# Optimization experiments

Hardware: AMD Instinct MI355X
Metric: run time of the kernel (lower is better)

The kernel has to match this reference:

```python
import jax, jax.numpy as jnp
import numpy as np

# dims
D_MODEL = 256; D_STATE = 16; D_CONV = 4; EXPAND = 2
D_INNER = D_MODEL * EXPAND            # 512
DT_RANK = 16                          # ceil(256/16)
B_SZ = 16; C_IN = 64; T_LR = 2560; R = 2; C_OUT = 64


def _p(key, shape, scale=0.02):
    return jax.random.normal(key, shape, jnp.float32) * scale


def setup_inputs() -> dict:
    key = jax.random.key(0)
    ks = iter(jax.random.split(key, 48))
    inp = {}
    inp['x'] = jax.random.normal(next(ks), (B_SZ, C_IN, T_LR), jnp.float32)
    # encoder: Conv1d(64->128,k3,p1) ; Conv1d(128->256,k3,p1)
    inp['enc_w1'] = _p(next(ks), (128, C_IN, 3)); inp['enc_b1'] = jnp.zeros((128,), jnp.float32)
    inp['enc_w2'] = _p(next(ks), (256, 128, 3)); inp['enc_b2'] = jnp.zeros((256,), jnp.float32)
    # BidirectionalMamba norms
    inp['norm1_w'] = jnp.ones((D_MODEL,), jnp.float32)
    inp['norm2_w'] = jnp.ones((D_MODEL,), jnp.float32)
    # one forward ('f') and one backward ('b') Mamba v1 block
    for p in ('f', 'b'):
        inp[p + '_inW'] = _p(next(ks), (2 * D_INNER, D_MODEL))
        inp[p + '_convW'] = _p(next(ks), (D_INNER, D_CONV), 0.2)
        inp[p + '_convb'] = jnp.zeros((D_INNER,), jnp.float32)
        inp[p + '_xW'] = _p(next(ks), (DT_RANK + 2 * D_STATE, D_INNER))
        inp[p + '_dtW'] = _p(next(ks), (D_INNER, DT_RANK), 0.1)
        inp[p + '_dtb'] = -4.0 + 2.0 * jax.random.uniform(next(ks), (D_INNER,), jnp.float32)
        inp[p + '_Alog'] = jnp.log(jnp.tile(jnp.arange(1, D_STATE + 1, dtype=jnp.float32), (D_INNER, 1)))
        inp[p + '_D'] = jnp.ones((D_INNER,), jnp.float32)
        inp[p + '_outW'] = _p(next(ks), (D_MODEL, D_INNER))
    # post-bottleneck: Conv1d(512->256,k3,p1) + BatchNorm1d(256) (eval)
    inp['convd_w'] = _p(next(ks), (256, 512, 3)); inp['convd_b'] = jnp.zeros((256,), jnp.float32)
    inp['bn_g'] = jnp.ones((256,), jnp.float32); inp['bn_b'] = jnp.zeros((256,), jnp.float32)
    inp['bn_mean'] = jnp.zeros((256,), jnp.float32); inp['bn_var'] = jnp.ones((256,), jnp.float32)
    # SubPixel1D: Conv1d(256 -> target_channels*r, k3, p1), r=2
    inp['sp_w'] = _p(next(ks), (C_OUT * R, 256, 3)); inp['sp_b'] = jnp.zeros((C_OUT * R,), jnp.float32)
    return inp


def silu(x):
    return x * jax.nn.sigmoid(x)


def conv1d(x, w, b):  # x: (B,C,L), w: (O,I,K), 'same' padding
    k = w.shape[-1]
    y = jax.lax.conv_general_dilated(x, w, (1,), [(k // 2, k // 2)],
                                     dimension_numbers=('NCH', 'OIH', 'NCH'))
    return y + b[None, :, None]


def rmsnorm(x, w, eps=1e-6):
    return x * jax.lax.rsqrt(jnp.mean(x * x, -1, keepdims=True) + eps) * w


def mamba(x, inW, convW, convb, xW, dtW, dtb, Alog, Dp, outW):
    # x: (B, L, D_MODEL) -> (B, L, D_MODEL); Mamba v1 selective scan.
    Bn = x.shape[0]
    xz = x @ inW.T                               # (B,L,2*di)
    xc, z = jnp.split(xz, 2, axis=-1)            # (B,L,di) each
    # causal depthwise conv over time
    xt = jnp.transpose(xc, (0, 2, 1))            # (B,di,L)
    xt = jax.lax.conv_general_dilated(xt, convW[:, None, :], (1,), [(D_CONV - 1, 0)],
                                      dimension_numbers=('NCH', 'OIH', 'NCH'),
                                      feature_group_count=D_INNER)
    xc = silu(jnp.transpose(xt + convb[None, :, None], (0, 2, 1)))  # (B,L,di)
    dbc = xc @ xW.T                              # (B,L,dt_rank+2N)
    dt = jax.nn.softplus(dbc[..., :DT_RANK] @ dtW.T + dtb)          # (B,L,di)
    Bc = dbc[..., DT_RANK:DT_RANK + D_STATE]     # (B,L,N)
    Cc = dbc[..., DT_RANK + D_STATE:]            # (B,L,N)
    A = -jnp.exp(Alog)                           # (di,N)

    def step(h, inp):
        dt_t, B_t, C_t, x_t = inp                # (B,di),(B,N),(B,N),(B,di)
        dA = jnp.exp(dt_t[..., None] * A)        # (B,di,N)
        h = dA * h + (dt_t * x_t)[..., None] * B_t[:, None, :]
        y = jnp.einsum('bdn,bn->bd', h, C_t)
        return h, y

    xs = (jnp.transpose(dt, (1, 0, 2)), jnp.transpose(Bc, (1, 0, 2)),
          jnp.transpose(Cc, (1, 0, 2)), jnp.transpose(xc, (1, 0, 2)))
    h0 = jnp.zeros((Bn, D_INNER, D_STATE), x.dtype)
    _, ys = jax.lax.scan(step, h0, xs)           # ys: (L,B,di)
    y = jnp.transpose(ys, (1, 0, 2)) + xc * Dp
    return (y * silu(z)) @ outW.T


def reference(x, enc_w1, enc_b1, enc_w2, enc_b2, norm1_w, norm2_w,
              f_inW, f_convW, f_convb, f_xW, f_dtW, f_dtb, f_Alog, f_D, f_outW,
              b_inW, b_convW, b_convb, b_xW, b_dtW, b_dtb, b_Alog, b_D, b_outW,
              convd_w, convd_b, bn_g, bn_b, bn_mean, bn_var, sp_w, sp_b):
    # encoder (dropout = identity in eval)
    e = silu(conv1d(x, enc_w1, enc_b1))
    e = silu(conv1d(e, enc_w2, enc_b2))          # (B,256,T)
    t = jnp.transpose(e, (0, 2, 1))              # (B,T,256)
    # Bi-Mamba bottleneck layer
    xn = rmsnorm(t, norm1_w)
    mo_f = mamba(xn, f_inW, f_convW, f_convb, f_xW, f_dtW, f_dtb, f_Alog, f_D, f_outW) + xn
    xb = xn[:, ::-1, :]
    mo_b = mamba(xb, b_inW, b_convW, b_convb, b_xW, b_dtW, b_dtb, b_Alog, b_D, b_outW) + xb
    mo_b = mo_b[:, ::-1, :]
    combined = rmsnorm(mo_f + mo_b, norm2_w)
    m = jnp.concatenate([combined, t], axis=-1)  # (B,T,512)
    m = jnp.transpose(m, (0, 2, 1))              # (B,512,T)
    # conv_d + BatchNorm1d (eval) + SiLU
    d = conv1d(m, convd_w, convd_b)
    d = (d - bn_mean[None, :, None]) * jax.lax.rsqrt(bn_var + 1e-5)[None, :, None] \
        * bn_g[None, :, None] + bn_b[None, :, None]
    d = silu(d)
    # SubPixel1D upsample x2
    s = conv1d(d, sp_w, sp_b)                    # (B, C_OUT*R, T)
    Bn, C, T = s.shape
    s = s.reshape(Bn, C // R, R, T).transpose(0, 1, 3, 2).reshape(Bn, C // R, T * R)
    return s                                      # (B, 64, 5120)
```

## Files before the change

### kernel.cpp

```cpp
#include <hip/hip_runtime.h>
#include <hip/hip_bf16.h>
#include <math.h>

#define B_SZ 16
#define T_LR 2560
#define BT (B_SZ * T_LR)
#define DM 256
#define DI 512
#define DS 16
#define DTR 16
#define CH 64
#define CH_LOG2 6
#define CLEN (T_LR / CH)

typedef __attribute__((ext_vector_type(8))) short bf16x8;
typedef __attribute__((ext_vector_type(4))) float f32x4;

__device__ __forceinline__ float silu_f(float x) {
    return x / (1.f + __expf(-x));
}
__device__ __forceinline__ unsigned short f2bf(float v) {
    __hip_bfloat16 h = __float2bfloat16(v);
    return *(unsigned short*)&h;
}
__device__ __forceinline__ float bf2f(unsigned short u) {
    union { unsigned int i; float f; } c;
    c.i = (unsigned int)u << 16;
    return c.f;
}
__device__ __forceinline__ int seqrev(int r) {
    int s = r / T_LR, t = r % T_LR;
    return s * T_LR + (T_LR - 1 - t);
}
__device__ __forceinline__ float softplus_f(float x) {
    return (x > 20.f) ? x : __logf(1.f + __expf(x));
}
__device__ __forceinline__ size_t wswz_idx(int tap, int n, int c, int N, int Kt) {
    return ((size_t)((tap * (N >> 4) + (n >> 4)) * (Kt >> 5) + (c >> 5)) << 9)
         + (size_t)((((c >> 3) & 3) * 16 + (n & 15)) * 8 + (c & 7));
}

__global__ __launch_bounds__(256) void k_prep(
    const float* __restrict__ enc_w1, const float* __restrict__ enc_w2,
    const float* __restrict__ convd_w, const float* __restrict__ sp_w,
    const float* __restrict__ convd_b, const float* __restrict__ bn_g,
    const float* __restrict__ bn_b, const float* __restrict__ bn_mean,
    const float* __restrict__ bn_var,
    const float* __restrict__ inW0, const float* __restrict__ inW1,
    const float* __restrict__ outW0, const float* __restrict__ outW1,
    const float* __restrict__ xW0, const float* __restrict__ xW1,
    const float* __restrict__ Alog0, const float* __restrict__ Alog1,
    const float* __restrict__ x,
    unsigned short* __restrict__ W1r, unsigned short* __restrict__ W2r,
    unsigned short* __restrict__ Wdr, unsigned short* __restrict__ Wspr,
    float* __restrict__ alpha, float* __restrict__ beta,
    unsigned short* __restrict__ inW_bf2, unsigned short* __restrict__ outW_bf2,
    unsigned short* __restrict__ xW_bc2, float* __restrict__ Aflag,
    unsigned short* __restrict__ xt)
{
    __shared__ float ts[32][33];
    __shared__ int s_ok;
    int blk = blockIdx.x;
    int tid = threadIdx.x;
    if (blk < 32) {
        int i = blk * 256 + tid;
        int n = i / 64, ci = i % 64;
        #pragma unroll
        for (int k = 0; k < 3; k++)
            W1r[wswz_idx(k, n, ci, 128, 64)] = f2bf(enc_w1[((size_t)n * 64 + ci) * 3 + k]);
    } else if (blk < 160) {
        int i = (blk - 32) * 256 + tid;
        int n = i / 128, ci = i % 128;
        #pragma unroll
        for (int k = 0; k < 3; k++)
            W2r[wswz_idx(k, n, ci, 256, 128)] = f2bf(enc_w2[((size_t)n * 128 + ci) * 3 + k]);
    } else if (blk < 672) {
        int i = (blk - 160) * 256 + tid;
        int n = i / 512, ci = i % 512;
        #pragma unroll
        for (int k = 0; k < 3; k++)
            Wdr[wswz_idx(k, n, ci, 256, 512)] = f2bf(convd_w[((size_t)n * 512 + ci) * 3 + k]);
    } else if (blk < 800) {
        int i = (blk - 672) * 256 + tid;
        int n = i / 256, ci = i % 256;
        #pragma unroll
        for (int k = 0; k < 3; k++)
            Wspr[wswz_idx(k, n, ci, 128, 256)] = f2bf(sp_w[((size_t)n * 256 + ci) * 3 + k]);
    } else if (blk < 801) {
        int c = tid;
        float a = bn_g[c] * rsqrtf(bn_var[c] + 1e-5f);
        alpha[c] = a;
        beta[c] = (convd_b[c] - bn_mean[c]) * a + bn_b[c];
    } else if (blk < 1825) {
        int i = (blk - 801) * 256 + tid;
        inW_bf2[i] = f2bf(inW0[i]);
        inW_bf2[262144 + i] = f2bf(inW1[i]);
    } else if (blk < 2337) {
        int i = (blk - 1825) * 256 + tid;
        outW_bf2[i] = f2bf(outW0[i]);
        outW_bf2[131072 + i] = f2bf(outW1[i]);
    } else if (blk < 2433) {
        int i = (blk - 2337) * 256 + tid;
        xW_bc2[i] = f2bf(xW0[i]);
        xW_bc2[24576 + i] = f2bf(xW1[i]);
    } else if (blk < 2434) {
        if (tid == 0) s_ok = 1;
        __syncthreads();
        int ok = 1;
        for (int i = tid; i < DI * DS; i += 256) {
            int d = i >> 4, n = i & 15;
            float a0f = __expf(Alog0[d * DS]);
            float anf = __expf(Alog0[d * DS + n]);
            if (fabsf(anf - (float)(n + 1) * a0f) > 1e-3f * (float)(n + 1)) ok = 0;
            float a0b = __expf(Alog1[d * DS]);
            float anb = __expf(Alog1[d * DS + n]);
            if (fabsf(anb - (float)(n + 1) * a0b) > 1e-3f * (float)(n + 1)) ok = 0;
        }
        if (!ok) atomicAnd(&s_ok, 0);
        __syncthreads();
        if (tid == 0) Aflag[0] = s_ok ? 1.f : 0.f;
    } else {
        int idx = blk - 2434;
        int t0 = (idx % 80) * 32;
        int c0 = ((idx / 80) & 1) * 32;
        int b = idx / 160;
        int tx = tid & 31, ty = tid >> 5;
        #pragma unroll
        for (int j = 0; j < 4; j++) {
            int c = c0 + ty + j * 8;
            ts[ty + j * 8][tx] = x[((size_t)b * 64 + c) * T_LR + t0 + tx];
        }
        __syncthreads();
        #pragma unroll
        for (int j = 0; j < 4; j++) {
            int t = t0 + ty + j * 8;
            xt[((size_t)b * T_LR + t) * 64 + c0 + tx] = f2bf(ts[tx][ty + j * 8]);
        }
    }
}

__global__ __launch_bounds__(256, 3) void k_conv3_bf(const unsigned short* __restrict__ A1, int K1,
                                                  const unsigned short* __restrict__ A2, int K2,
                                                  const unsigned short* __restrict__ Wz,
                                                  const float* __restrict__ alpha,
                                                  const float* __restrict__ beta,
                                                  float* __restrict__ outf,
                                                  unsigned short* __restrict__ outb,
                                                  int N, int dosilu, int pixsh) {
    int Kt = K1 + K2;
    __shared__ __align__(16) unsigned short smem[2 * 130 * 40];
    unsigned short (*As)[130][40] = (unsigned short (*)[130][40])smem;
    float* sC = (float*)smem;
    int tid = threadIdx.x;
    int wave = tid >> 6, lane = tid & 63;
    int wm = (wave >> 1) * 64, wn = (wave & 1) * 64;
    int m0 = blockIdx.x * 128, n0 = blockIdx.y * 128;
    int b = m0 / T_LR, t0 = m0 % T_LR;
    int q = lane >> 4, ml = lane & 15;
    int Nb16 = N >> 4, Kb32 = Kt >> 5;
    int nb0 = (n0 + wn) >> 4;
    const unsigned short* wl = Wz + (size_t)lane * 8;
    f32x4 acc[4][4] = {};
    int cq = tid & 3;
    int r0 = tid >> 2;
    int r1 = r0 + 64;
    int r2 = r0 + 128;
    bool has2 = (tid < 8);
    int ta0 = t0 - 1 + r0, ta1 = t0 - 1 + r1, ta2 = t0 - 1 + r2;
    bool va0 = (ta0 >= 0) && (ta0 < T_LR);
    bool va1 = (ta1 < T_LR);
    bool va2 = has2 && (ta2 < T_LR);
    uint4 v0, v1, v2;
    #define LOADA(vv, valid, t, col) { vv = make_uint4(0u,0u,0u,0u); if (valid) { \
        const unsigned short* src = ((col) < K1) \
            ? A1 + (size_t)(b * T_LR + (t)) * K1 + (col) \
            : A2 + (size_t)(b * T_LR + (t)) * K2 + ((col) - K1); \
        vv = *(const uint4*)src; } }
    LOADA(v0, va0, ta0, cq * 8);
    LOADA(v1, va1, ta1, cq * 8);
    LOADA(v2, va2, ta2, cq * 8);
    *(uint4*)&As[0][r0][cq * 8] = v0;
    *(uint4*)&As[0][r1][cq * 8] = v1;
    if (has2) *(uint4*)&As[0][r2][cq * 8] = v2;
    int nk = Kb32;
    for (int kk = 0; kk < nk; kk++) {
        __syncthreads();
        int cur = kk & 1;
        if (kk + 1 < nk) {
            int col = ((kk + 1) << 5) + cq * 8;
            LOADA(v0, va0, ta0, col);
            LOADA(v1, va1, ta1, col);
            LOADA(v2, va2, ta2, col);
        }
        #pragma unroll
        for (int tap = 0; tap < 3; tap++) {
            int tb = tap * Nb16 + nb0;
            bf16x8 bfr[4];
            #pragma unroll
            for (int ni = 0; ni < 4; ni++)
                bfr[ni] = *(const bf16x8*)(wl + ((size_t)((tb + ni) * Kb32 + kk) << 9));
            #pragma unroll
            for (int mi = 0; mi < 4; mi++) {
                bf16x8 af = *(const bf16x8*)&As[cur][wm + mi * 16 + ml + tap][q * 8];
                #pragma unroll
                for (int ni = 0; ni < 4; ni++)
                    acc[mi][ni] = __builtin_amdgcn_mfma_f32_16x16x32_bf16(af, bfr[ni], acc[mi][ni], 0, 0, 0);
            }
        }
        if (kk + 1 < nk) {
            *(uint4*)&As[cur ^ 1][r0][cq * 8] = v0;
            *(uint4*)&As[cur ^ 1][r1][cq * 8] = v1;
            if (has2) *(uint4*)&As[cur ^ 1][r2][cq * 8] = v2;
        }
    }
    #undef LOADA
    int rowoff = m0 - b * T_LR;
    #pragma unroll
    for (int p = 0; p < 4; p++) {
        __syncthreads();
        if ((wave >> 1) == (p >> 1)) {
            int mib = (p & 1) * 2;
            #pragma unroll
            for (int m2 = 0; m2 < 2; m2++) {
                int mi = mib + m2;
                int rl = mi * 16 + q * 4 - (p & 1) * 32;
                #pragma unroll
                for (int r = 0; r < 4; r++)
                    #pragma unroll
                    for (int ni = 0; ni < 4; ni++)
                        sC[(rl + r) * 140 + wn + ni * 16 + ml] = acc[mi][ni][r];
            }
        }
        __syncthreads();
        if (pixsh) {
            int row = tid & 31, c2g = tid >> 5;
            int t = rowoff + p * 32 + row;
            float* dst = outf + ((size_t)b * 64 * T_LR + t) * 2;
            #pragma unroll
            for (int j = 0; j < 8; j++) {
                int c2 = c2g + j * 8;
                float va = sC[row * 140 + 2 * c2]     + beta[2 * c2];
                float vb = sC[row * 140 + 2 * c2 + 1] + beta[2 * c2 + 1];
                *(float2*)&dst[(size_t)c2 * T_LR * 2] = make_float2(va, vb);
            }
        } else {
            #pragma unroll
            for (int gi = 0; gi < 2; gi++) {
                int g = tid + gi * 256;
                int row = g >> 4;
                int colg = (g & 15) * 8;
                int mr = m0 + p * 32 + row;
                const float* src = sC + row * 140 + colg;
                float vv[8];
                *(float4*)&vv[0] = *(const float4*)src;
                *(float4*)&vv[4] = *(const float4*)(src + 4);
                unsigned short ob[8];
                #pragma unroll
                for (int jj = 0; jj < 8; jj++) {
                    int col = n0 + colg + jj;
                    float a = alpha ? alpha[col] : 1.f;
                    float v = vv[jj] * a + beta[col];
                    if (dosilu) v = silu_f(v);
                    vv[jj] = v;
                    ob[jj] = f2bf(v);
                }
                if (outf) {
                    *(float4*)(outf + (size_t)mr * N + n0 + colg) = *(float4*)&vv[0];
                    *(float4*)(outf + (size_t)mr * N + n0 + colg + 4) = *(float4*)&vv[4];
                }
                if (outb)
                    *(uint4*)(outb + (size_t)mr * N + n0 + colg) = *(uint4*)ob;
            }
        }
    }
}

__global__ __launch_bounds__(256) void k_inproj_conv(const unsigned short* __restrict__ xn,
                                                     const unsigned short* __restrict__ inW2,
                                                     const float* __restrict__ cw0,
                                                     const float* __restrict__ cw1,
                                                     const float* __restrict__ cb0,
                                                     const float* __restrict__ cb1,
                                                     unsigned short* __restrict__ xcs,
                                                     long long dsXcs) {
    __shared__ unsigned short As[128][40];
    __shared__ unsigned short Bs[128][40];
    __shared__ unsigned short Ct[131][136];
    int dir = blockIdx.z;
    int arev = dir;
    const unsigned short* inW = inW2 + (size_t)dir * 1024 * DM;
    const float* cw = dir ? cw1 : cw0;
    const float* cb = dir ? cb1 : cb0;
    xcs += (size_t)dir * dsXcs;
    int tid = threadIdx.x;
    int wave = tid >> 6, lane = tid & 63;
    int wm = (wave >> 1) * 64, wn = (wave & 1) * 64;
    int m0 = blockIdx.x * 128, n0 = blockIdx.y * 128;
    int b = m0 / T_LR, t0 = m0 % T_LR;
    int sc = tid & 3, sr = tid >> 2;
    int ar0 = m0 + sr, ar1 = m0 + sr + 64;
    if (arev) { ar0 = seqrev(ar0); ar1 = seqrev(ar1); }
    const unsigned short* ap0 = xn + (size_t)ar0 * DM + sc * 8;
    const unsigned short* ap1 = xn + (size_t)ar1 * DM + sc * 8;
    const unsigned short* bp0 = inW + (size_t)(n0 + sr) * DM + sc * 8;
    const unsigned short* bp1 = inW + (size_t)(n0 + sr + 64) * DM + sc * 8;
    f32x4 acc[4][4] = {};
    int q = lane >> 4, ml = lane & 15;
    for (int k0 = 0; k0 < DM; k0 += 32) {
        uint4 a0 = *(const uint4*)(ap0 + k0);
        uint4 a1 = *(const uint4*)(ap1 + k0);
        uint4 b0 = *(const uint4*)(bp0 + k0);
        uint4 b1 = *(const uint4*)(bp1 + k0);
        __syncthreads();
        *(uint4*)&As[sr][sc * 8]      = a0;
        *(uint4*)&As[sr + 64][sc * 8] = a1;
        *(uint4*)&Bs[sr][sc * 8]      = b0;
        *(uint4*)&Bs[sr + 64][sc * 8] = b1;
        __syncthreads();
        bf16x8 af[4], bfr[4];
        #pragma unroll
        for (int mi = 0; mi < 4; mi++)
            af[mi] = *(const bf16x8*)&As[wm + mi * 16 + ml][q * 8];
        #pragma unroll
        for (int ni = 0; ni < 4; ni++)
            bfr[ni] = *(const bf16x8*)&Bs[wn + ni * 16 + ml][q * 8];
        #pragma unroll
        for (int mi = 0; mi < 4; mi++)
            #pragma unroll
            for (int ni = 0; ni < 4; ni++)
                acc[mi][ni] = __builtin_amdgcn_mfma_f32_16x16x32_bf16(af[mi], bfr[ni], acc[mi][ni], 0, 0, 0);
    }
    #pragma unroll
    for (int mi = 0; mi < 4; mi++)
        #pragma unroll
        for (int r = 0; r < 4; r++)
            #pragma unroll
            for (int ni = 0; ni < 4; ni++)
                Ct[3 + wm + mi * 16 + q * 4 + r][wn + ni * 16 + ml] = f2bf(acc[mi][ni][r]);
    for (int i = tid; i < 384; i += 256) {
        int hr = i >> 7, c = i & 127;
        int tr = t0 - 3 + hr;
        float v = 0.f;
        if (tr >= 0) {
            int src = b * T_LR + (arev ? (T_LR - 1 - tr) : tr);
            const unsigned short* xr = xn + (size_t)src * DM;
            const unsigned short* wr = inW + (size_t)(n0 + c) * DM;
            for (int k = 0; k < DM; k += 8) {
                uint4 xa = *(const uint4*)(xr + k);
                uint4 wa = *(const uint4*)(wr + k);
                const unsigned short* xs = (const unsigned short*)&xa;
                const unsigned short* wsp = (const unsigned short*)&wa;
                #pragma unroll
                for (int j = 0; j < 8; j++) v += bf2f(xs[j]) * bf2f(wsp[j]);
            }
        }
        Ct[hr][c] = f2bf(v);
    }
    __syncthreads();
    int col = tid & 127;
    int d = n0 + col;
    float w0 = cw[d * 4 + 0], w1 = cw[d * 4 + 1], w2 = cw[d * 4 + 2], w3 = cw[d * 4 + 3];
    float bi = cb[d];
    int rbase = tid >> 7;
    for (int j = 0; j < 64; j++) {
        int row = rbase + 2 * j;
        float v = bi + bf2f(Ct[row][col]) * w0 + bf2f(Ct[row + 1][col]) * w1
                     + bf2f(Ct[row + 2][col]) * w2 + bf2f(Ct[row + 3][col]) * w3;
        xcs[(size_t)(m0 + row) * DI + d] = f2bf(silu_f(v));
    }
}

__global__ __launch_bounds__(256) void k_rmsnorm(const float* __restrict__ in1,
                                                 const float* __restrict__ in2,
                                                 const float* __restrict__ w,
                                                 float* __restrict__ out,
                                                 unsigned short* __restrict__ out_bf,
                                                 int ntok) {
    int tok = (blockIdx.x * 256 + threadIdx.x) >> 6;
    int lane = threadIdx.x & 63;
    if (tok >= ntok) return;
    float4 v = ((const float4*)(in1 + (size_t)tok * DM))[lane];
    if (in2) {
        float4 u = ((const float4*)(in2 + (size_t)tok * DM))[lane];
        v.x += u.x; v.y += u.y; v.z += u.z; v.w += u.w;
    }
    float ss = v.x * v.x + v.y * v.y + v.z * v.z + v.w * v.w;
    #pragma unroll
    for (int off = 32; off > 0; off >>= 1) ss += __shfl_xor(ss, off);
    float sc = rsqrtf(ss * (1.f / 256.f) + 1e-6f);
    float4 wv = ((const float4*)w)[lane];
    float4 o;
    o.x = v.x * sc * wv.x; o.y = v.y * sc * wv.y;
    o.z = v.z * sc * wv.z; o.w = v.w * sc * wv.w;
    if (out) ((float4*)(out + (size_t)tok * DM))[lane] = o;
    if (out_bf) {
        ushort4 ob;
        ob.x = f2bf(o.x); ob.y = f2bf(o.y); ob.z = f2bf(o.z); ob.w = f2bf(o.w);
        ((ushort4*)(out_bf + (size_t)tok * DM))[lane] = ob;
    }
}

__global__ __launch_bounds__(256) void k_gemm_bf(const unsigned short* __restrict__ A, int lda, long long dsA,
                                                 const unsigned short* __restrict__ Bw, long long dsB,
                                                 float* Cf, long long dsCf, int ldc,
                                                 const float* __restrict__ res,
                                                 int K, int Nout, int crevmode) {
    __shared__ unsigned short As[128][40];
    __shared__ unsigned short Bs[128][40];
    int dir = blockIdx.z;
    A += (long long)dir * dsA;
    Bw += (long long)dir * dsB;
    Cf += (long long)dir * dsCf;
    int crev = (crevmode == 2) ? dir : crevmode;
    int tid = threadIdx.x;
    int wave = tid >> 6, lane = tid & 63;
    int wm = (wave >> 1) * 64, wn = (wave & 1) * 64;
    int m0 = blockIdx.x * 128, n0 = blockIdx.y * 128;
    int sc = tid & 3, sr = tid >> 2;
    const unsigned short* ap0 = A + (size_t)(m0 + sr) * lda + sc * 8;
    const unsigned short* ap1 = A + (size_t)(m0 + sr + 64) * lda + sc * 8;
    bool bv0 = (n0 + sr) < Nout;
    bool bv1 = (n0 + sr + 64) < Nout;
    const unsigned short* bp0 = Bw + (size_t)(n0 + sr) * K + sc * 8;
    const unsigned short* bp1 = Bw + (size_t)(n0 + sr + 64) * K + sc * 8;
    f32x4 acc[4][4] = {};
    int q = lane >> 4, ml = lane & 15;
    for (int k0 = 0; k0 < K; k0 += 32) {
        uint4 a0 = *(const uint4*)(ap0 + k0);
        uint4 a1 = *(const uint4*)(ap1 + k0);
        uint4 b0 = make_uint4(0u, 0u, 0u, 0u), b1 = make_uint4(0u, 0u, 0u, 0u);
        if (bv0) b0 = *(const uint4*)(bp0 + k0);
        if (bv1) b1 = *(const uint4*)(bp1 + k0);
        __syncthreads();
        *(uint4*)&As[sr][sc * 8]      = a0;
        *(uint4*)&As[sr + 64][sc * 8] = a1;
        *(uint4*)&Bs[sr][sc * 8]      = b0;
        *(uint4*)&Bs[sr + 64][sc * 8] = b1;
        __syncthreads();
        bf16x8 af[4], bfr[4];
        #pragma unroll
        for (int mi = 0; mi < 4; mi++)
            af[mi] = *(const bf16x8*)&As[wm + mi * 16 + ml][q * 8];
        #pragma unroll
        for (int ni = 0; ni < 4; ni++)
            bfr[ni] = *(const bf16x8*)&Bs[wn + ni * 16 + ml][q * 8];
        #pragma unroll
        for (int mi = 0; mi < 4; mi++)
            #pragma unroll
            for (int ni = 0; ni < 4; ni++)
                acc[mi][ni] = __builtin_amdgcn_mfma_f32_16x16x32_bf16(af[mi], bfr[ni], acc[mi][ni], 0, 0, 0);
    }
    #pragma unroll
    for (int mi = 0; mi < 4; mi++) {
        #pragma unroll
        for (int r = 0; r < 4; r++) {
            int mr = m0 + wm + mi * 16 + q * 4 + r;
            int orow = crev ? seqrev(mr) : mr;
            #pragma unroll
            for (int ni = 0; ni < 4; ni++) {
                int col = n0 + wn + ni * 16 + ml;
                if (col < Nout) {
                    float v = acc[mi][ni][r];
                    if (res) v += res[(size_t)orow * ldc + col];
                    Cf[(size_t)orow * ldc + col] = v;
                }
            }
        }
    }
}

__global__ __launch_bounds__(256) void k_gemm_bf_cb(const unsigned short* __restrict__ A, int lda,
                                                    const unsigned short* __restrict__ Bw, long long dsB,
                                                    unsigned short* __restrict__ Cb, int ldc, long long dsCb,
                                                    const unsigned short* __restrict__ gate, long long dsGate,
                                                    int K) {
    __shared__ __align__(16) unsigned short smem[2 * 128 * 40];
    unsigned short (*As)[40] = (unsigned short(*)[40])smem;
    unsigned short (*Bs)[40] = (unsigned short(*)[40])(smem + 128 * 40);
    float* sC = (float*)smem;
    int dir = blockIdx.z;
    int arev = dir;
    Bw += (long long)dir * dsB;
    Cb += (long long)dir * dsCb;
    gate += (long long)dir * dsGate;
    int tid = threadIdx.x;
    int wave = tid >> 6, lane = tid & 63;
    int wm = (wave >> 1) * 64, wn = (wave & 1) * 64;
    int m0 = blockIdx.x * 128, n0 = blockIdx.y * 128;
    int sc = tid & 3, sr = tid >> 2;
    int ar0 = m0 + sr, ar1 = m0 + sr + 64;
    if (arev) { ar0 = seqrev(ar0); ar1 = seqrev(ar1); }
    const unsigned short* ap0 = A + (size_t)ar0 * lda + sc * 8;
    const unsigned short* ap1 = A + (size_t)ar1 * lda + sc * 8;
    const unsigned short* bp0 = Bw + (size_t)(n0 + sr) * K + sc * 8;
    const unsigned short* bp1 = Bw + (size_t)(n0 + sr + 64) * K + sc * 8;
    f32x4 acc[4][4] = {};
    int q = lane >> 4, ml = lane & 15;
    for (int k0 = 0; k0 < K; k0 += 32) {
        uint4 a0 = *(const uint4*)(ap0 + k0);
        uint4 a1 = *(const uint4*)(ap1 + k0);
        uint4 b0 = *(const uint4*)(bp0 + k0);
        uint4 b1 = *(const uint4*)(bp1 + k0);
        __syncthreads();
        *(uint4*)&As[sr][sc * 8]      = a0;
        *(uint4*)&As[sr + 64][sc * 8] = a1;
        *(uint4*)&Bs[sr][sc * 8]      = b0;
        *(uint4*)&Bs[sr + 64][sc * 8] = b1;
        __syncthreads();
        bf16x8 af[4], bfr[4];
        #pragma unroll
        for (int mi = 0; mi < 4; mi++)
            af[mi] = *(const bf16x8*)&As[wm + mi * 16 + ml][q * 8];
        #pragma unroll
        for (int ni = 0; ni < 4; ni++)
            bfr[ni] = *(const bf16x8*)&Bs[wn + ni * 16 + ml][q * 8];
        #pragma unroll
        for (int mi = 0; mi < 4; mi++)
            #pragma unroll
            for (int ni = 0; ni < 4; ni++)
                acc[mi][ni] = __builtin_amdgcn_mfma_f32_16x16x32_bf16(af[mi], bfr[ni], acc[mi][ni], 0, 0, 0);
    }
    #pragma unroll
    for (int p = 0; p < 4; p++) {
        __syncthreads();
        if ((wave >> 1) == (p >> 1)) {
            int mib = (p & 1) * 2;
            #pragma unroll
            for (int m2 = 0; m2 < 2; m2++) {
                int mi = mib + m2;
                int rl = mi * 16 + q * 4 - (p & 1) * 32;
                #pragma unroll
                for (int r = 0; r < 4; r++)
                    #pragma unroll
                    for (int ni = 0; ni < 4; ni++)
                        sC[(rl + r) * 140 + wn + ni * 16 + ml] = acc[mi][ni][r];
            }
        }
        __syncthreads();
        #pragma unroll
        for (int gi = 0; gi < 2; gi++) {
            int g = tid + gi * 256;
            int row = g >> 4;
            int colg = (g & 15) * 8;
            int grow = m0 + p * 32 + row;
            const float* src = sC + row * 140 + colg;
            float4 v0 = *(const float4*)src;
            float4 v1 = *(const float4*)(src + 4);
            float vv[8] = {v0.x, v0.y, v0.z, v0.w, v1.x, v1.y, v1.z, v1.w};
            unsigned short gu[8];
            *(uint4*)gu = *(const uint4*)(gate + (size_t)grow * ldc + n0 + colg);
            unsigned short o[8];
            #pragma unroll
            for (int jj = 0; jj < 8; jj++) {
                float v = vv[jj];
                v = silu_f(v) * bf2f(gu[jj]);
                o[jj] = f2bf(v);
            }
            *(uint4*)(Cb + (size_t)grow * ldc + n0 + colg) = *(uint4*)o;
        }
    }
}

__global__ __launch_bounds__(256) void k_scan_p1(const unsigned short* __restrict__ x,
                                                 const float* __restrict__ db,
                                                 const float* __restrict__ dtW0, const float* __restrict__ dtW1,
                                                 const float* __restrict__ dtb0, const float* __restrict__ dtb1,
                                                 const float* __restrict__ Alog0, const float* __restrict__ Alog1,
                                                 const float* __restrict__ Aflag,
                                                 float* __restrict__ hS,
                                                 float* __restrict__ csum, int Bc) {
    __shared__ float dbs[CLEN * 48];
    int tid = threadIdx.x;
    int gid = blockIdx.x * 256 + tid;
    int d = gid & (DI - 1);
    int bcix = gid >> 9;
    int c = bcix & (CH - 1);
    int bl = bcix >> CH_LOG2;
    int dir = (bl >= Bc) ? 1 : 0;
    const float* dtW  = dir ? dtW1  : dtW0;
    const float* dtb  = dir ? dtb1  : dtb0;
    const float* Alog = dir ? Alog1 : Alog0;
    int tbase = c * CLEN;
    const float* dbp = db + ((size_t)bl * T_LR + tbase) * 48;
    for (int i = tid; i < (CLEN * 48) / 4; i += 256)
        *(float4*)&dbs[i * 4] = *(const float4*)(dbp + i * 4);
    bool fast = (Aflag[0] != 0.f);
    float A0 = -__expf(Alog[d * DS]);
    float Av[DS], h[DS];
    #pragma unroll
    for (int n = 0; n < DS; n++) h[n] = 0.f;
    if (!fast) {
        #pragma unroll
        for (int n = 0; n < DS; n++) Av[n] = -__expf(Alog[d * DS + n]);
    }
    const float4* wp = (const float4*)(dtW + d * 16);
    float4 w0 = wp[0], w1 = wp[1], w2 = wp[2], w3 = wp[3];
    float bias = dtb[d];
    const unsigned short* xp = x + ((size_t)bl * T_LR + tbase) * DI + d;
    float S = 0.f;
    __syncthreads();
    for (int t = 0; t < CLEN; t++) {
        const float* bc = dbs + t * 48;
        float dl = bias
            + bc[0] * w0.x + bc[1] * w0.y + bc[2] * w0.z + bc[3] * w0.w
            + bc[4] * w1.x + bc[5] * w1.y + bc[6] * w1.z + bc[7] * w1.w
            + bc[8] * w2.x + bc[9] * w2.y + bc[10] * w2.z + bc[11] * w2.w
            + bc[12] * w3.x + bc[13] * w3.y + bc[14] * w3.z + bc[15] * w3.w;
        float dtv = softplus_f(dl);
        float xv  = bf2f(xp[(size_t)t * DI]);
        float dtx = dtv * xv;
        S += dtv;
        if (fast) {
            float e1 = __expf(dtv * A0);
            float e = e1;
            #pragma unroll
            for (int n = 0; n < DS; n++) {
                h[n] = e * h[n] + dtx * bc[16 + n];
                e *= e1;
            }
        } else {
            #pragma unroll
            for (int n = 0; n < DS; n++)
                h[n] = __expf(dtv * Av[n]) * h[n] + dtx * bc[16 + n];
        }
    }
    float* hp = hS + (size_t)gid * DS;
    #pragma unroll
    for (int n = 0; n < DS; n++) hp[n] = h[n];
    csum[gid] = S;
}

__global__ __launch_bounds__(256) void k_scan_p2(float* __restrict__ hS,
                                                 const float* __restrict__ csum,
                                                 const float* __restrict__ Alog0,
                                                 const float* __restrict__ Alog1, int Bc) {
    int gid = blockIdx.x * 256 + threadIdx.x;
    int n = gid & (DS - 1);
    int d = (gid >> 4) & (DI - 1);
    int bl = gid >> 13;
    const float* Alog = (bl >= Bc) ? Alog1 : Alog0;
    float An = -__expf(Alog[d * DS + n]);
    float hs = 0.f;
    for (int c = 0; c < CH; c++) {
        size_t base = ((size_t)(bl * CH + c) * DI + d);
        float he = hS[base * DS + n];
        float S  = csum[base];
        hS[base * DS + n] = hs;
        hs = __expf(An * S) * hs + he;
    }
}

__global__ __launch_bounds__(256) void k_scan_p3(unsigned short* __restrict__ x,
                                                 const float* __restrict__ db,
                                                 const float* __restrict__ dtW0, const float* __restrict__ dtW1,
                                                 const float* __restrict__ dtb0, const float* __restrict__ dtb1,
                                                 const float* __restrict__ Alog0, const float* __restrict__ Alog1,
                                                 const float* __restrict__ Aflag,
                                                 const float* __restrict__ Dp0, const float* __restrict__ Dp1,
                                                 const float* __restrict__ hS, int Bc) {
    __shared__ float dbs[CLEN * 48];
    int tid = threadIdx.x;
    int gid = blockIdx.x * 256 + tid;
    int d = gid & (DI - 1);
    int bcix = gid >> 9;
    int c = bcix & (CH - 1);
    int bl = bcix >> CH_LOG2;
    int dir = (bl >= Bc) ? 1 : 0;
    const float* dtW  = dir ? dtW1  : dtW0;
    const float* dtb  = dir ? dtb1  : dtb0;
    const float* Alog = dir ? Alog1 : Alog0;
    const float* Dp   = dir ? Dp1   : Dp0;
    int tbase = c * CLEN;
    const float* dbp = db + ((size_t)bl * T_LR + tbase) * 48;
    for (int i = tid; i < (CLEN * 48) / 4; i += 256)
        *(float4*)&dbs[i * 4] = *(const float4*)(dbp + i * 4);
    bool fast = (Aflag[0] != 0.f);
    float A0 = -__expf(Alog[d * DS]);
    float Av[DS], h[DS];
    const float* hp = hS + (size_t)gid * DS;
    #pragma unroll
    for (int n = 0; n < DS; n++) h[n] = hp[n];
    if (!fast) {
        #pragma unroll
        for (int n = 0; n < DS; n++) Av[n] = -__expf(Alog[d * DS + n]);
    }
    const float4* wp = (const float4*)(dtW + d * 16);
    float4 w0 = wp[0], w1 = wp[1], w2 = wp[2], w3 = wp[3];
    float bias = dtb[d];
    float Dd = Dp[d];
    unsigned short* xp = x + ((size_t)bl * T_LR + tbase) * DI + d;
    __syncthreads();
    for (int t = 0; t < CLEN; t++) {
        const float* bc = dbs + t * 48;
        float dl = bias
            + bc[0] * w0.x + bc[1] * w0.y + bc[2] * w0.z + bc[3] * w0.w
            + bc[4] * w1.x + bc[5] * w1.y + bc[6] * w1.z + bc[7] * w1.w
            + bc[8] * w2.x + bc[9] * w2.y + bc[10] * w2.z + bc[11] * w2.w
            + bc[12] * w3.x + bc[13] * w3.y + bc[14] * w3.z + bc[15] * w3.w;
        float dtv = softplus_f(dl);
        float xv  = bf2f(xp[(size_t)t * DI]);
        float dtx = dtv * xv;
        float acc = 0.f;
        if (fast) {
            float e1 = __expf(dtv * A0);
            float e = e1;
            #pragma unroll
            for (int n = 0; n < DS; n++) {
                h[n] = e * h[n] + dtx * bc[16 + n];
                acc += h[n] * bc[32 + n];
                e *= e1;
            }
        } else {
            #pragma unroll
            for (int n = 0; n < DS; n++) {
                h[n] = __expf(dtv * Av[n]) * h[n] + dtx * bc[16 + n];
                acc += h[n] * bc[32 + n];
            }
        }
        xp[(size_t)t * DI] = f2bf(acc + xv * Dd);
    }
}

extern "C" void kernel_launch(void* const* d_in, const int* in_sizes, int n_in,
                              void* d_out, int out_size, void* d_ws, size_t ws_size,
                              hipStream_t stream) {
    const float* x       = (const float*)d_in[0];
    const float* enc_w1  = (const float*)d_in[1];
    const float* enc_b1  = (const float*)d_in[2];
    const float* enc_w2  = (const float*)d_in[3];
    const float* enc_b2  = (const float*)d_in[4];
    const float* norm1_w = (const float*)d_in[5];
    const float* norm2_w = (const float*)d_in[6];
    const float* convd_w = (const float*)d_in[25];
    const float* convd_b = (const float*)d_in[26];
    const float* bn_g    = (const float*)d_in[27];
    const float* bn_b    = (const float*)d_in[28];
    const float* bn_mean = (const float*)d_in[29];
    const float* bn_var  = (const float*)d_in[30];
    const float* sp_w    = (const float*)d_in[31];
    const float* sp_b    = (const float*)d_in[32];
    float* out = (float*)d_out;

    const float* inW0   = (const float*)d_in[7];
    const float* cw0    = (const float*)d_in[8];
    const float* cb0    = (const float*)d_in[9];
    const float* xW0    = (const float*)d_in[10];
    const float* dtW0   = (const float*)d_in[11];
    const float* dtb0   = (const float*)d_in[12];
    const float* Alog0  = (const float*)d_in[13];
    const float* Dp0    = (const float*)d_in[14];
    const float* outW0  = (const float*)d_in[15];
    const float* inW1   = (const float*)d_in[16];
    const float* cw1    = (const float*)d_in[17];
    const float* cb1    = (const float*)d_in[18];
    const float* xW1    = (const float*)d_in[19];
    const float* dtW1   = (const float*)d_in[20];
    const float* dtb1   = (const float*)d_in[21];
    const float* Alog1  = (const float*)d_in[22];
    const float* Dp1    = (const float*)d_in[23];
    const float* outW1  = (const float*)d_in[24];

    float* ws = (float*)d_ws;
    size_t availf = ws_size / sizeof(float);
    size_t o = 0;
    float* t_buf  = ws + o; o += (size_t)BT * DM;
    float* xn_buf = ws + o; o += (size_t)BT * DM;
    float* mo     = ws + o; o += (size_t)BT * DM;
    unsigned short* xn_bf = (unsigned short*)(ws + o); o += (size_t)BT * DM / 2;
    unsigned short* tb_bf = (unsigned short*)(ws + o); o += (size_t)BT * DM / 2;
    unsigned short* inW_bf2  = (unsigned short*)(ws + o); o += (size_t)1024 * DM;
    unsigned short* outW_bf2 = (unsigned short*)(ws + o); o += (size_t)DM * DI;
    unsigned short* xW_bc2   = (unsigned short*)(ws + o); o += (size_t)48 * DI;
    unsigned short* W1r  = (unsigned short*)(ws + o); o += (3 * 128 * 64) / 2;
    unsigned short* W2r  = (unsigned short*)(ws + o); o += (3 * 256 * 128) / 2;
    unsigned short* Wdr  = (unsigned short*)(ws + o); o += (3 * 256 * 512) / 2;
    unsigned short* Wspr = (unsigned short*)(ws + o); o += (3 * 128 * 256) / 2;
    float* alpha_d = ws + o; o += 256;
    float* beta_d  = ws + o; o += 256;
    float* Aflag_d = ws + o; o += 4;
    size_t persist = o;
    float* scratch = ws + persist;
    size_t scratch_avail = (availf > persist) ? (availf - persist) : 0;
    size_t per_b2 = 2 * ((size_t)T_LR * DI / 2 * 2 + (size_t)T_LR * 48
                         + (size_t)CH * DI * (DS + 1));
    int Bc = 16;
    while (Bc > 1 && (size_t)Bc * per_b2 > scratch_avail) Bc >>= 1;

    unsigned short* xt  = (unsigned short*)mo;
    unsigned short* e1t = (unsigned short*)(mo + (size_t)BT * 64 / 2);
    unsigned short* comb_bf = (unsigned short*)xn_buf;
    unsigned short* d_bf = (unsigned short*)mo;

    k_prep<<<4994, 256, 0, stream>>>(enc_w1, enc_w2, convd_w, sp_w,
                                     convd_b, bn_g, bn_b, bn_mean, bn_var,
                                     inW0, inW1, outW0, outW1, xW0, xW1,
                                     Alog0, Alog1,
                                     x, W1r, W2r, Wdr, Wspr, alpha_d, beta_d,
                                     inW_bf2, outW_bf2, xW_bc2, Aflag_d, xt);

    k_conv3_bf<<<dim3(BT / 128, 1), 256, 0, stream>>>(xt, 64, nullptr, 0, W1r,
                                                      nullptr, enc_b1, nullptr, e1t, 128, 1, 0);
    k_conv3_bf<<<dim3(BT / 128, 2), 256, 0, stream>>>(e1t, 128, nullptr, 0, W2r,
                                                      nullptr, enc_b2, t_buf, tb_bf, 256, 1, 0);
    k_rmsnorm<<<BT / 4, 256, 0, stream>>>(t_buf, nullptr, norm1_w, xn_buf, xn_bf, BT);

    long long dsMo1 = (long long)(t_buf - mo);
    for (int b0 = 0; b0 < B_SZ; b0 += Bc) {
        int Tc = Bc * T_LR;
        long long TcDI = (long long)Tc * DI;
        unsigned short* xcs = (unsigned short*)scratch;
        unsigned short* ygb = xcs + (size_t)2 * Tc * DI;
        float* db   = (float*)(ygb + (size_t)2 * Tc * DI);
        float* hS   = db + (size_t)2 * Tc * 48;
        float* csum = hS + (size_t)2 * Bc * CH * DI * DS;
        const float*          xnC  = xn_buf + (size_t)b0 * T_LR * DM;
        const unsigned short* xnbC = xn_bf  + (size_t)b0 * T_LR * DM;
        float*                moC  = mo     + (size_t)b0 * T_LR * DM;
        k_inproj_conv<<<dim3(Tc / 128, DI / 128, 2), 256, 0, stream>>>(
            xnbC, inW_bf2, cw0, cw1, cb0, cb1, xcs, TcDI);
        k_gemm_bf<<<dim3(Tc / 128, 1, 2), 256, 0, stream>>>(
            xcs, DI, TcDI, xW_bc2, (long long)48 * DI,
            db, (long long)Tc * 48, 48, nullptr, DI, 48, 0);
        k_scan_p1<<<(2 * Bc * CH * DI) / 256, 256, 0, stream>>>(
            xcs, db, dtW0, dtW1, dtb0, dtb1, Alog0, Alog1, Aflag_d, hS, csum, Bc);
        k_scan_p2<<<(2 * Bc * DI * DS) / 256, 256, 0, stream>>>(
            hS, csum, Alog0, Alog1, Bc);
        k_scan_p3<<<(2 * Bc * CH * DI) / 256, 256, 0, stream>>>(
            xcs, db, dtW0, dtW1, dtb0, dtb1, Alog0, Alog1, Aflag_d, Dp0, Dp1, hS, Bc);
        k_gemm_bf_cb<<<dim3(Tc / 128, DI / 128, 2), 256, 0, stream>>>(
            xnbC, DM, inW_bf2 + (size_t)DI * DM, (long long)1024 * DM,
            ygb, DI, TcDI, xcs, TcDI, DM);
        k_gemm_bf<<<dim3(Tc / 128, DM / 128, 2), 256, 0, stream>>>(
            ygb, DI, TcDI, outW_bf2, (long long)DM * DI,
            moC, dsMo1, DM, xnC, DI, DM, 2);
    }

    k_rmsnorm<<<BT / 4, 256, 0, stream>>>(mo, t_buf, norm2_w, nullptr, comb_bf, BT);
    k_conv3_bf<<<dim3(BT / 128, 2), 256, 0, stream>>>(comb_bf, 256, tb_bf, 256, Wdr,
                                                      alpha_d, beta_d, nullptr, d_bf, 256, 1, 0);
    k_conv3_bf<<<dim3(BT / 128, 1), 256, 0, stream>>>(d_bf, 256, nullptr, 0, Wspr,
                                                      nullptr, sp_b, out, nullptr, 128, 0, 1);
}
```

Baseline: 1.156 ms.

## Compute z half of in-projection in conv kernel, apply SiLU gate in scan

The in-projection kernel now covers all 1024 output columns. Blocks in the upper half write the raw z projection as bf16 to a buffer. The separate gated GEMM kernel, which recomputed z and multiplied silu(z) into y, is removed. The gate is applied inside scan phase 3, which writes y*silu(z) straight into xcs for the out-projection. This cuts one kernel launch and the ygb round trip, at the cost of an extra z buffer write and read. It also adds a divergent branch in the in-projection kernel.

```diff
diff --git a/kernel.cpp b/kernel.cpp
--- a/kernel.cpp
+++ b/kernel.cpp
@@ -282,6 +282,7 @@
                                                      const float* __restrict__ cb0,
                                                      const float* __restrict__ cb1,
                                                      unsigned short* __restrict__ xcs,
+                                                     unsigned short* __restrict__ zb,
                                                      long long dsXcs) {
     __shared__ unsigned short As[128][40];
     __shared__ unsigned short Bs[128][40];
@@ -289,9 +290,8 @@
     int dir = blockIdx.z;
     int arev = dir;
     const unsigned short* inW = inW2 + (size_t)dir * 1024 * DM;
-    const float* cw = dir ? cw1 : cw0;
-    const float* cb = dir ? cb1 : cb0;
     xcs += (size_t)dir * dsXcs;
+    zb  += (size_t)dir * dsXcs;
     int tid = threadIdx.x;
     int wave = tid >> 6, lane = tid & 63;
     int wm = (wave >> 1) * 64, wn = (wave & 1) * 64;
@@ -330,43 +330,69 @@
             for (int ni = 0; ni < 4; ni++)
                 acc[mi][ni] = __builtin_amdgcn_mfma_f32_16x16x32_bf16(af[mi], bfr[ni], acc[mi][ni], 0, 0, 0);
     }
-    #pragma unroll
-    for (int mi = 0; mi < 4; mi++)
-        #pragma unroll
-        for (int r = 0; r < 4; r++)
-            #pragma unroll
-            for (int ni = 0; ni < 4; ni++)
-                Ct[3 + wm + mi * 16 + q * 4 + r][wn + ni * 16 + ml] = f2bf(acc[mi][ni][r]);
-    for (int i = tid; i < 384; i += 256) {
-        int hr = i >> 7, c = i & 127;
-        int tr = t0 - 3 + hr;
-        float v = 0.f;
-        if (tr >= 0) {
-            int src = b * T_LR + (arev ? (T_LR - 1 - tr) : tr);
-            const unsigned short* xr = xn + (size_t)src * DM;
-            const unsigned short* wr = inW + (size_t)(n0 + c) * DM;
-            for (int k = 0; k < DM; k += 8) {
-                uint4 xa = *(const uint4*)(xr + k);
-                uint4 wa = *(const uint4*)(wr + k);
-                const unsigned short* xs = (const unsigned short*)&xa;
-                const unsigned short* wsp = (const unsigned short*)&wa;
+    if (n0 < DI) {
+        const float* cw = dir ? cw1 : cw0;
+        const float* cb = dir ? cb1 : cb0;
+        #pragma unroll
+        for (int mi = 0; mi < 4; mi++)
+            #pragma unroll
+            for (int r = 0; r < 4; r++)
                 #pragma unroll
-                for (int j = 0; j < 8; j++) v += bf2f(xs[j]) * bf2f(wsp[j]);
-            }
-        }
-        Ct[hr][c] = f2bf(v);
-    }
-    __syncthreads();
-    int col = tid & 127;
-    int d = n0 + col;
-    float w0 = cw[d * 4 + 0], w1 = cw[d * 4 + 1], w2 = cw[d * 4 + 2], w3 = cw[d * 4 + 3];
-    float bi = cb[d];
-    int rbase = tid >> 7;
-    for (int j = 0; j < 64; j++) {
-        int row = rbase + 2 * j;
-        float v = bi + bf2f(Ct[row][col]) * w0 + bf2f(Ct[row + 1][col]) * w1
-                     + bf2f(Ct[row + 2][col]) * w2 + bf2f(Ct[row + 3][col]) * w3;
-        xcs[(size_t)(m0 + row) * DI + d] = f2bf(silu_f(v));
+                for (int ni = 0; ni < 4; ni++)
+                    Ct[3 + wm + mi * 16 + q * 4 + r][wn + ni * 16 + ml] = f2bf(acc[mi][ni][r]);
+        for (int i = tid; i < 384; i += 256) {
+            int hr = i >> 7, c = i & 127;
+            int tr = t0 - 3 + hr;
+            float v = 0.f;
+            if (tr >= 0) {
+                int src = b * T_LR + (arev ? (T_LR - 1 - tr) : tr);
+                const unsigned short* xr = xn + (size_t)src * DM;
+                const unsigned short* wr = inW + (size_t)(n0 + c) * DM;
+                for (int k = 0; k < DM; k += 8) {
+                    uint4 xa = *(const uint4*)(xr + k);
+                    uint4 wa = *(const uint4*)(wr + k);
+                    const unsigned short* xs = (const unsigned short*)&xa;
+                    const unsigned short* wsp = (const unsigned short*)&wa;
+                    #pragma unroll
+                    for (int j = 0; j < 8; j++) v += bf2f(xs[j]) * bf2f(wsp[j]);
+                }
+            }
+            Ct[hr][c] = f2bf(v);
+        }
+        __syncthreads();
+        int col = tid & 127;
+        int d = n0 + col;
+        float w0 = cw[d * 4 + 0], w1 = cw[d * 4 + 1], w2 = cw[d * 4 + 2], w3 = cw[d * 4 + 3];
+        float bi = cb[d];
+        int rbase = tid >> 7;
+        for (int j = 0; j < 64; j++) {
+            int row = rbase + 2 * j;
+            float v = bi + bf2f(Ct[row][col]) * w0 + bf2f(Ct[row + 1][col]) * w1
+                         + bf2f(Ct[row + 2][col]) * w2 + bf2f(Ct[row + 3][col]) * w3;
+            xcs[(size_t)(m0 + row) * DI + d] = f2bf(silu_f(v));
+        }
+    } else {
+        #pragma unroll
+        for (int mi = 0; mi < 4; mi++)
+            #pragma unroll
+            for (int r = 0; r < 4; r++)
+                #pragma unroll
+                for (int ni = 0; ni < 4; ni++)
+                    Ct[wm + mi * 16 + q * 4 + r][wn + ni * 16 + ml] = f2bf(acc[mi][ni][r]);
+        __syncthreads();
+        int zc0 = n0 - DI;
+        #pragma unroll
+        for (int gi = 0; gi < 2; gi++) {
+            int g = tid + gi * 256;
+            int row = g >> 2;
+            int colg = (g & 3) * 32;
+            unsigned short* dst = zb + (size_t)(m0 + row) * DI + zc0 + colg;
+            const unsigned short* srcc = &Ct[row][colg];
+            *(uint4*)(dst)      = *(const uint4*)(srcc);
+            *(uint4*)(dst + 8)  = *(const uint4*)(srcc + 8);
+            *(uint4*)(dst + 16) = *(const uint4*)(srcc + 16);
+            *(uint4*)(dst + 24) = *(const uint4*)(srcc + 24);
+        }
     }
 }
 
@@ -469,98 +495,6 @@
     }
 }
 
-__global__ __launch_bounds__(256) void k_gemm_bf_cb(const unsigned short* __restrict__ A, int lda,
-                                                    const unsigned short* __restrict__ Bw, long long dsB,
-                                                    unsigned short* __restrict__ Cb, int ldc, long long dsCb,
-                                                    const unsigned short* __restrict__ gate, long long dsGate,
-                                                    int K) {
-    __shared__ __align__(16) unsigned short smem[2 * 128 * 40];
-    unsigned short (*As)[40] = (unsigned short(*)[40])smem;
-    unsigned short (*Bs)[40] = (unsigned short(*)[40])(smem + 128 * 40);
-    float* sC = (float*)smem;
-    int dir = blockIdx.z;
-    int arev = dir;
-    Bw += (long long)dir * dsB;
-    Cb += (long long)dir * dsCb;
-    gate += (long long)dir * dsGate;
-    int tid = threadIdx.x;
-    int wave = tid >> 6, lane = tid & 63;
-    int wm = (wave >> 1) * 64, wn = (wave & 1) * 64;
-    int m0 = blockIdx.x * 128, n0 = blockIdx.y * 128;
-    int sc = tid & 3, sr = tid >> 2;
-    int ar0 = m0 + sr, ar1 = m0 + sr + 64;
-    if (arev) { ar0 = seqrev(ar0); ar1 = seqrev(ar1); }
-    const unsigned short* ap0 = A + (size_t)ar0 * lda + sc * 8;
-    const unsigned short* ap1 = A + (size_t)ar1 * lda + sc * 8;
-    const unsigned short* bp0 = Bw + (size_t)(n0 + sr) * K + sc * 8;
-    const unsigned short* bp1 = Bw + (size_t)(n0 + sr + 64) * K + sc * 8;
-    f32x4 acc[4][4] = {};
-    int q = lane >> 4, ml = lane & 15;
-    for (int k0 = 0; k0 < K; k0 += 32) {
-        uint4 a0 = *(const uint4*)(ap0 + k0);
-        uint4 a1 = *(const uint4*)(ap1 + k0);
-        uint4 b0 = *(const uint4*)(bp0 + k0);
-        uint4 b1 = *(const uint4*)(bp1 + k0);
-        __syncthreads();
-        *(uint4*)&As[sr][sc * 8]      = a0;
-        *(uint4*)&As[sr + 64][sc * 8] = a1;
-        *(uint4*)&Bs[sr][sc * 8]      = b0;
-        *(uint4*)&Bs[sr + 64][sc * 8] = b1;
-        __syncthreads();
-        bf16x8 af[4], bfr[4];
-        #pragma unroll
-        for (int mi = 0; mi < 4; mi++)
-            af[mi] = *(const bf16x8*)&As[wm + mi * 16 + ml][q * 8];
-        #pragma unroll
-        for (int ni = 0; ni < 4; ni++)
-            bfr[ni] = *(const bf16x8*)&Bs[wn + ni * 16 + ml][q * 8];
-        #pragma unroll
-        for (int mi = 0; mi < 4; mi++)
-            #pragma unroll
-            for (int ni = 0; ni < 4; ni++)
-                acc[mi][ni] = __builtin_amdgcn_mfma_f32_16x16x32_bf16(af[mi], bfr[ni], acc[mi][ni], 0, 0, 0);
-    }
-    #pragma unroll
-    for (int p = 0; p < 4; p++) {
-        __syncthreads();
-        if ((wave >> 1) == (p >> 1)) {
-            int mib = (p & 1) * 2;
-            #pragma unroll
-            for (int m2 = 0; m2 < 2; m2++) {
-                int mi = mib + m2;
-                int rl = mi * 16 + q * 4 - (p & 1) * 32;
-                #pragma unroll
-                for (int r = 0; r < 4; r++)
-                    #pragma unroll
-                    for (int ni = 0; ni < 4; ni++)
-                        sC[(rl + r) * 140 + wn + ni * 16 + ml] = acc[mi][ni][r];
-            }
-        }
-        __syncthreads();
-        #pragma unroll
-        for (int gi = 0; gi < 2; gi++) {
-            int g = tid + gi * 256;
-            int row = g >> 4;
-            int colg = (g & 15) * 8;
-            int grow = m0 + p * 32 + row;
-            const float* src = sC + row * 140 + colg;
-            float4 v0 = *(const float4*)src;
-            float4 v1 = *(const float4*)(src + 4);
-            float vv[8] = {v0.x, v0.y, v0.z, v0.w, v1.x, v1.y, v1.z, v1.w};
-            unsigned short gu[8];
-            *(uint4*)gu = *(const uint4*)(gate + (size_t)grow * ldc + n0 + colg);
-            unsigned short o[8];
-            #pragma unroll
-            for (int jj = 0; jj < 8; jj++) {
-                float v = vv[jj];
-                v = silu_f(v) * bf2f(gu[jj]);
-                o[jj] = f2bf(v);
-            }
-            *(uint4*)(Cb + (size_t)grow * ldc + n0 + colg) = *(uint4*)o;
-        }
-    }
-}
-
 __global__ __launch_bounds__(256) void k_scan_p1(const unsigned short* __restrict__ x,
                                                  const float* __restrict__ db,
                                                  const float* __restrict__ dtW0, const float* __restrict__ dtW1,
@@ -651,6 +585,7 @@
 }
 
 __global__ __launch_bounds__(256) void k_scan_p3(unsigned short* __restrict__ x,
+                                                 const unsigned short* __restrict__ zb,
                                                  const float* __restrict__ db,
                                                  const float* __restrict__ dtW0, const float* __restrict__ dtW1,
                                                  const float* __restrict__ dtb0, const float* __restrict__ dtb1,
@@ -689,6 +624,7 @@
     float bias = dtb[d];
     float Dd = Dp[d];
     unsigned short* xp = x + ((size_t)bl * T_LR + tbase) * DI + d;
+    const unsigned short* zp = zb + ((size_t)bl * T_LR + tbase) * DI + d;
     __syncthreads();
     for (int t = 0; t < CLEN; t++) {
         const float* bc = dbs + t * 48;
@@ -717,7 +653,9 @@
                 acc += h[n] * bc[32 + n];
             }
         }
-        xp[(size_t)t * DI] = f2bf(acc + xv * Dd);
+        float yv = acc + xv * Dd;
+        float zv = bf2f(zp[(size_t)t * DI]);
+        xp[(size_t)t * DI] = f2bf(silu_f(zv) * yv);
     }
 }
 
@@ -809,15 +747,15 @@
         int Tc = Bc * T_LR;
         long long TcDI = (long long)Tc * DI;
         unsigned short* xcs = (unsigned short*)scratch;
-        unsigned short* ygb = xcs + (size_t)2 * Tc * DI;
-        float* db   = (float*)(ygb + (size_t)2 * Tc * DI);
+        unsigned short* zb  = xcs + (size_t)2 * Tc * DI;
+        float* db   = (float*)(zb + (size_t)2 * Tc * DI);
         float* hS   = db + (size_t)2 * Tc * 48;
         float* csum = hS + (size_t)2 * Bc * CH * DI * DS;
         const float*          xnC  = xn_buf + (size_t)b0 * T_LR * DM;
         const unsigned short* xnbC = xn_bf  + (size_t)b0 * T_LR * DM;
         float*                moC  = mo     + (size_t)b0 * T_LR * DM;
-        k_inproj_conv<<<dim3(Tc / 128, DI / 128, 2), 256, 0, stream>>>(
-            xnbC, inW_bf2, cw0, cw1, cb0, cb1, xcs, TcDI);
+        k_inproj_conv<<<dim3(Tc / 128, 1024 / 128, 2), 256, 0, stream>>>(
+            xnbC, inW_bf2, cw0, cw1, cb0, cb1, xcs, zb, TcDI);
         k_gemm_bf<<<dim3(Tc / 128, 1, 2), 256, 0, stream>>>(
             xcs, DI, TcDI, xW_bc2, (long long)48 * DI,
             db, (long long)Tc * 48, 48, nullptr, DI, 48, 0);
@@ -826,12 +764,9 @@
         k_scan_p2<<<(2 * Bc * DI * DS) / 256, 256, 0, stream>>>(
             hS, csum, Alog0, Alog1, Bc);
         k_scan_p3<<<(2 * Bc * CH * DI) / 256, 256, 0, stream>>>(
-            xcs, db, dtW0, dtW1, dtb0, dtb1, Alog0, Alog1, Aflag_d, Dp0, Dp1, hS, Bc);
-        k_gemm_bf_cb<<<dim3(Tc / 128, DI / 128, 2), 256, 0, stream>>>(
-            xnbC, DM, inW_bf2 + (size_t)DI * DM, (long long)1024 * DM,
-            ygb, DI, TcDI, xcs, TcDI, DM);
+            xcs, zb, db, dtW0, dtW1, dtb0, dtb1, Alog0, Alog1, Aflag_d, Dp0, Dp1, hS, Bc);
         k_gemm_bf<<<dim3(Tc / 128, DM / 128, 2), 256, 0, stream>>>(
-            ygb, DI, TcDI, outW_bf2, (long long)DM * DI,
+            xcs, DI, TcDI, outW_bf2, (long long)DM * DI,
             moC, dsMo1, DM, xnC, DI, DM, 2);
     }
 
```

Result: faster. 1.113 ms (-3.7%).
